# Optimization experiments

Measured on AMD Instinct MI355X. Metric: run time of the kernel, lower is better.

The kernel has to match this reference:

```python
import jax, jax.numpy as jnp
import numpy as np
from jax import lax

B, S, E, H = 8, 1024, 1024, 16
HEAD_DIM = E // H
THRESHOLD = 0.5
NEG_FILL = -1e9


def setup_inputs() -> dict:
    key = jax.random.key(0)
    k0, k1, k2 = jax.random.split(key, 3)
    x = jax.random.normal(k0, (B, S, E), jnp.float32)
    in_proj_w = jax.random.normal(k1, (3 * E, E), jnp.float32) * 0.02
    in_proj_b = jnp.zeros((3 * E,), jnp.float32)
    out_proj_w = jax.random.normal(k2, (E, E), jnp.float32) * 0.02
    out_proj_b = jnp.zeros((E,), jnp.float32)
    return {"x": x, "in_proj_w": in_proj_w, "in_proj_b": in_proj_b,
            "out_proj_w": out_proj_w, "out_proj_b": out_proj_b}


def _mha(x, in_proj_w, in_proj_b, out_proj_w, out_proj_b):
    # PyTorch nn.MultiheadAttention with q=k=v=x, batch_first=True
    qkv = x @ in_proj_w.T + in_proj_b                     # [B,S,3E]
    q, k, v = jnp.split(qkv, 3, axis=-1)                  # each [B,S,E]
    def split_heads(t):
        return t.reshape(B, S, H, HEAD_DIM).transpose(0, 2, 1, 3)  # [B,H,S,d]
    q, k, v = split_heads(q), split_heads(k), split_heads(v)
    scale = 1.0 / np.sqrt(HEAD_DIM).astype(np.float32)
    scores = jnp.einsum('bhqd,bhkd->bhqk', q, k) * scale  # [B,H,S,S]
    w = jax.nn.softmax(scores, axis=-1)
    o = jnp.einsum('bhqk,bhkd->bhqd', w, v)               # [B,H,S,d]
    o = o.transpose(0, 2, 1, 3).reshape(B, S, E)
    attn_output = o @ out_proj_w.T + out_proj_b           # [B,S,E]
    attn_weights = w.mean(axis=1)                         # head-averaged [B,S,S]
    return attn_output, attn_weights


def _cluster(attn_weights):
    # Sequential greedy clustering: scan rows i in order; if row i is not yet
    # visited, its high-attention columns (> THRESHOLD) form cluster i and are
    # marked visited. cluster_id[b, j] = row index of the first cluster that
    # claimed token j, or -1 if never claimed.
    visited0 = jnp.zeros((B, S), dtype=bool)
    cid0 = jnp.full((B, S), -1, dtype=jnp.int32)

    def step(carry, i):
        visited, cid = carry
        process = ~jnp.take(visited, i, axis=1)           # [B] row i unvisited?
        high = jnp.take(attn_weights, i, axis=1) > THRESHOLD  # [B,S]
        claimed = process[:, None] & high                 # [B,S]
        newly = claimed & (~visited)
        cid = jnp.where(newly, jnp.int32(i), cid)
        visited = visited | claimed
        return (visited, cid), None

    (visited, cid), _ = lax.scan(step, (visited0, cid0), jnp.arange(S))
    return cid, visited


def reference(x, in_proj_w, in_proj_b, out_proj_w, out_proj_b):
    attn_output, attn_weights = _mha(x, in_proj_w, in_proj_b, out_proj_w, out_proj_b)
    cluster_ids, covered = _cluster(attn_weights)
    # _generate_image_features: x where token belongs to some cluster, -1e9 else
    clustered_outputs = jnp.where(covered[..., None], x, jnp.float32(NEG_FILL))
    return attn_output, attn_weights, clustered_outputs, cluster_ids
```

## Files before the change

kernel.cpp:

```cpp
#include <hip/hip_runtime.h>
#include <hip/hip_bf16.h>

#define B 8
#define S 1024
#define E 1024
#define H 16

typedef unsigned short u16;
typedef unsigned char u8;
typedef unsigned int u32;
typedef unsigned long long u64;

typedef __attribute__((ext_vector_type(8))) short s16x8;
typedef __attribute__((ext_vector_type(4))) float f32x4;
typedef __attribute__((ext_vector_type(16))) float f32x16;

__device__ __forceinline__ float bf2f(u16 u) {
    union { u32 i; float f; } x; x.i = ((u32)u) << 16; return x.f;
}
__device__ __forceinline__ u16 f2bf(float f) {
    union { float f; u32 i; } x; x.f = f;
    u32 r = x.i + 0x7FFFu + ((x.i >> 16) & 1u);
    return (u16)(r >> 16);
}
__device__ __forceinline__ f32x16 zero16() {
    f32x16 z;
#pragma unroll
    for (int i = 0; i < 16; ++i) z[i] = 0.f;
    return z;
}
__device__ __forceinline__ void gload16(const u16* g, u16* l) {
    __builtin_amdgcn_global_load_lds(
        (const __attribute__((address_space(1))) u32*)g,
        (__attribute__((address_space(3))) u32*)l, 16, 0, 0);
}

__global__ __launch_bounds__(256) void cvt_all(
    const float* __restrict__ x, const float* __restrict__ w0,
    const float* __restrict__ w1, u16* __restrict__ xb,
    u16* __restrict__ wb0, u16* __restrict__ wb1) {
    int i = blockIdx.x * 256 + threadIdx.x;
    const float* src;
    u16* dst;
    int off;
    if (i < 2097152) { src = x; dst = xb; off = i; }
    else if (i < 2883584) { src = w0; dst = wb0; off = i - 2097152; }
    else { src = w1; dst = wb1; off = i - 2883584; }
    float4 v = ((const float4*)src)[off];
    union { u16 u[4]; ushort4 s; } p;
    p.u[0] = f2bf(v.x); p.u[1] = f2bf(v.y);
    p.u[2] = f2bf(v.z); p.u[3] = f2bf(v.w);
    ((ushort4*)dst)[off] = p.s;
}

template <int MODE>
__global__ __launch_bounds__(256) void mfma_gemm(
    const u16* __restrict__ A, const u16* __restrict__ W,
    const float* __restrict__ bias, u16* __restrict__ qb, u16* __restrict__ kb,
    u16* __restrict__ vt, float* __restrict__ outf) {
    __shared__ __align__(16) u16 smem[16384];
    u16* As = smem;
    u16* Bs = smem + 8192;
    const int t = threadIdx.x;
    const int lane = t & 63;
    const int w = t >> 6;
    const int lin = (int)(blockIdx.y * gridDim.x + blockIdx.x);
    const int xcd = lin & 7;
    const int idx = lin >> 3;
    int mt, nt;
    if (MODE == 0) { mt = (xcd & 3) * 16 + (idx & 15); nt = (xcd >> 2) * 12 + (idx >> 4); }
    else           { mt = xcd * 8 + (idx & 7);         nt = idx >> 3; }
    const int m0 = mt * 128;
    const int n0 = nt * 128;
    const int wm = w >> 1, wn = w & 1;
    const int l15 = lane & 15, l4 = lane >> 4;
    const int lr = lane >> 3;
    const int lc = ((lane & 7) ^ lr) * 8;

    f32x4 acc[4][4];
#pragma unroll
    for (int i = 0; i < 4; ++i)
#pragma unroll
        for (int j = 0; j < 4; ++j) acc[i][j] = {0.f, 0.f, 0.f, 0.f};

    for (int k0 = 0; k0 < 1024; k0 += 64) {
        __syncthreads();
#pragma unroll
        for (int jj = 0; jj < 4; ++jj) {
            int j = w * 4 + jj;
            gload16(A + (size_t)(m0 + j * 8 + lr) * 1024 + k0 + lc, As + j * 512);
            gload16(W + (size_t)(n0 + j * 8 + lr) * 1024 + k0 + lc, Bs + j * 512);
        }
        __syncthreads();
#pragma unroll
        for (int ks = 0; ks < 2; ++ks) {
            s16x8 af[4], bf[4];
#pragma unroll
            for (int i = 0; i < 4; ++i) {
                int row = wm * 64 + i * 16 + l15;
                af[i] = *(const s16x8*)((const u8*)As +
                        (((row << 7) + (ks << 6) + (l4 << 4)) ^ ((row & 7) << 4)));
            }
#pragma unroll
            for (int j = 0; j < 4; ++j) {
                int row = wn * 64 + j * 16 + l15;
                bf[j] = *(const s16x8*)((const u8*)Bs +
                        (((row << 7) + (ks << 6) + (l4 << 4)) ^ ((row & 7) << 4)));
            }
#pragma unroll
            for (int i = 0; i < 4; ++i)
#pragma unroll
                for (int j = 0; j < 4; ++j)
                    acc[i][j] = __builtin_amdgcn_mfma_f32_16x16x32_bf16(
                        af[i], bf[j], acc[i][j], 0, 0, 0);
        }
    }

    if (MODE == 0) {
        __syncthreads();
        u16* Cs = smem;
        const int seg = n0 >> 10;
        const int bb = m0 >> 10;
        const int ms = m0 & 1023;
        if (seg < 2) {
            const float sc = (seg == 0) ? 0.18033688011f : 1.0f;
#pragma unroll
            for (int j = 0; j < 4; ++j) {
                int nl = wn * 64 + j * 16 + l15;
                float bn = bias[n0 + nl];
#pragma unroll
                for (int i = 0; i < 4; ++i) {
                    int ml = wm * 64 + i * 16 + l4 * 4;
#pragma unroll
                    for (int rr = 0; rr < 4; ++rr)
                        Cs[(ml + rr) * 128 + nl] = f2bf((acc[i][j][rr] + bn) * sc);
                }
            }
            __syncthreads();
            u16* dst0 = (seg == 0) ? qb : kb;
#pragma unroll
            for (int it = 0; it < 8; ++it) {
                int flat = it * 256 + t;
                int ml = flat >> 4;
                int g = (flat >> 3) & 1;
                int c8 = flat & 7;
                int hh = ((n0 + g * 64) & 1023) >> 6;
                u16* dst = dst0 + (((size_t)(bb * 16 + hh) * 1024 + ms + ml) << 6) + c8 * 8;
                *(uint4*)dst = *(const uint4*)(Cs + ml * 128 + g * 64 + c8 * 8);
            }
        } else {
#pragma unroll
            for (int j = 0; j < 4; ++j) {
                int nl = wn * 64 + j * 16 + l15;
                float bn = bias[n0 + nl];
                int sz = (nl & 7) << 4;
#pragma unroll
                for (int i = 0; i < 4; ++i) {
                    int ml = wm * 64 + i * 16 + l4 * 4;
#pragma unroll
                    for (int rr = 0; rr < 4; ++rr) {
                        int bl = (ml + rr) << 1;
                        *(u16*)((u8*)Cs + (nl << 8) + (bl ^ sz)) =
                            f2bf(acc[i][j][rr] + bn);
                    }
                }
            }
            __syncthreads();
#pragma unroll
            for (int it = 0; it < 8; ++it) {
                int flat = it * 256 + t;
                int nl = flat >> 4;
                int c = flat & 15;
                int n = n0 + nl;
                int hh = (n & 1023) >> 6;
                int d = n & 63;
                u16* dst = vt + ((size_t)(bb * 16 + hh) * 64 + d) * 1024 + ms + c * 8;
                *(uint4*)dst = *(const uint4*)((u8*)Cs + (nl << 8) +
                                               ((c << 4) ^ ((nl & 7) << 4)));
            }
        }
    } else {
#pragma unroll
        for (int j = 0; j < 4; ++j) {
            int n = n0 + wn * 64 + j * 16 + l15;
            float bn = bias[n];
#pragma unroll
            for (int i = 0; i < 4; ++i) {
                int mbase = m0 + wm * 64 + i * 16 + l4 * 4;
#pragma unroll
                for (int rr = 0; rr < 4; ++rr)
                    outf[(size_t)(mbase + rr) * 1024 + n] = acc[i][j][rr] + bn;
            }
        }
    }
}

template <int BASE>
__device__ __forceinline__ s16x8 build_pa(f32x16 e) {
    u32 a, bv, c, d;
    asm("v_cvt_pk_bf16_f32 %0, %1, %2" : "=v"(a) : "v"(e[BASE + 0]), "v"(e[BASE + 1]));
    asm("v_cvt_pk_bf16_f32 %0, %1, %2" : "=v"(bv) : "v"(e[BASE + 2]), "v"(e[BASE + 3]));
    asm("v_cvt_pk_bf16_f32 %0, %1, %2" : "=v"(c) : "v"(e[BASE + 4]), "v"(e[BASE + 5]));
    asm("v_cvt_pk_bf16_f32 %0, %1, %2" : "=v"(d) : "v"(e[BASE + 6]), "v"(e[BASE + 7]));
    asm("v_permlane32_swap_b32 %0, %1" : "+v"(a), "+v"(c));
    asm("v_permlane32_swap_b32 %0, %1" : "+v"(bv), "+v"(d));
    union { u32 w[4]; s16x8 v; } u;
    u.w[0] = a; u.w[1] = bv; u.w[2] = c; u.w[3] = d;
    return u.v;
}
__device__ __forceinline__ float pair_max(float v) {
    float a_ = v, b_ = v;
    asm("v_permlane32_swap_b32 %0, %1" : "+v"(a_), "+v"(b_));
    return fmaxf(a_, b_);
}
__device__ __forceinline__ float pair_sum(float v) {
    float a_ = v, b_ = v;
    asm("v_permlane32_swap_b32 %0, %1" : "+v"(a_), "+v"(b_));
    return a_ + b_;
}
__device__ __forceinline__ u32 pair_or(u32 v) {
    u32 a_ = v, b_ = v;
    asm("v_permlane32_swap_b32 %0, %1" : "+v"(a_), "+v"(b_));
    return a_ | b_;
}

__global__ __launch_bounds__(256, 4) void attn_flash(
    const u16* __restrict__ qg, const u16* __restrict__ kg,
    const u16* __restrict__ vtg, u16* __restrict__ og,
    float* __restrict__ stats) {
    __shared__ __align__(16) u16 bufK[2][64 * 64];
    __shared__ __align__(16) u16 bufV[2][64 * 64];
    const int t = threadIdx.x;
    const int lane = t & 63;
    const int w = t >> 6;
    const int task = ((blockIdx.x & 7) << 7) | (blockIdx.x >> 3);
    const int b = task >> 7;
    const int h = (task >> 3) & 15;
    const int qg_ = task & 7;
    const int q = lane & 31;
    const int hi = lane >> 5;
    const int q0 = qg_ * 128 + w * 32;
    const size_t hb = (size_t)(b * 16 + h) << 16;

    const int lr = lane >> 3;
    const int lc = ((lane & 7) ^ lr) * 8;
    const int swz = (q & 7) << 4;

#define STAGE(tt, bb)                                                          \
    do {                                                                       \
        _Pragma("unroll") for (int jj = 0; jj < 2; ++jj) {                     \
            int j = w * 2 + jj;                                                \
            gload16(kg + hb + (size_t)((tt) * 64 + j * 8 + lr) * 64 + lc,      \
                    bufK[bb] + j * 512);                                       \
            gload16(vtg + hb + (size_t)(j * 8 + lr) * 1024 + (tt) * 64 + lc,   \
                    bufV[bb] + j * 512);                                       \
        }                                                                      \
    } while (0)

    s16x8 qf[4];
#pragma unroll
    for (int s = 0; s < 4; ++s)
        qf[s] = *(const s16x8*)(qg + hb + (size_t)(q0 + q) * 64 + s * 16 + hi * 8);

    f32x16 oLo = zero16(), oHi = zero16();
    float m = -1e30f, l = 0.f;

    STAGE(0, 0);
    __syncthreads();
    int cur = 0;

    for (int tile = 0; tile < 16; ++tile) {
        if (tile < 15) STAGE(tile + 1, cur ^ 1);
        const u16* bK = bufK[cur];
        const u16* bV = bufV[cur];
#pragma unroll
        for (int kk = 0; kk < 64; kk += 32) {
            s16x8 ka[4];
#pragma unroll
            for (int s = 0; s < 4; ++s)
                ka[s] = *(const s16x8*)((const u8*)bK +
                        ((((kk + q) << 7) + (s << 5) + (hi << 4)) ^ swz));
            f32x16 s_ = zero16();
#pragma unroll
            for (int s = 0; s < 4; ++s)
                s_ = __builtin_amdgcn_mfma_f32_32x32x16_bf16(ka[s], qf[s], s_, 0, 0, 0);
            float m0 = fmaxf(fmaxf(s_[0], s_[4]), fmaxf(s_[8], s_[12]));
            float m1 = fmaxf(fmaxf(s_[1], s_[5]), fmaxf(s_[9], s_[13]));
            float m2 = fmaxf(fmaxf(s_[2], s_[6]), fmaxf(s_[10], s_[14]));
            float m3 = fmaxf(fmaxf(s_[3], s_[7]), fmaxf(s_[11], s_[15]));
            float pmax = pair_max(fmaxf(fmaxf(m0, m1), fmaxf(m2, m3)));
            if (__any(pmax > m + 11.5f)) {
                float mn = fmaxf(m, pmax);
                float r = exp2f(m - mn);
                m = mn;
                l *= r;
                oLo = oLo * r;
                oHi = oHi * r;
            }
            float s0 = 0.f, s1 = 0.f, s2 = 0.f, s3 = 0.f;
#pragma unroll
            for (int i = 0; i < 16; i += 4) {
                s_[i + 0] = exp2f(s_[i + 0] - m);
                s_[i + 1] = exp2f(s_[i + 1] - m);
                s_[i + 2] = exp2f(s_[i + 2] - m);
                s_[i + 3] = exp2f(s_[i + 3] - m);
                s0 += s_[i + 0]; s1 += s_[i + 1]; s2 += s_[i + 2]; s3 += s_[i + 3];
            }
            l += pair_sum((s0 + s1) + (s2 + s3));
            s16x8 p0 = build_pa<0>(s_), p1 = build_pa<8>(s_);
            s16x8 vLo0 = *(const s16x8*)((const u8*)bV +
                         (((q << 7) + (kk << 1) + (hi << 4)) ^ swz));
            s16x8 vLo1 = *(const s16x8*)((const u8*)bV +
                         (((q << 7) + (kk << 1) + 32 + (hi << 4)) ^ swz));
            s16x8 vHi0 = *(const s16x8*)((const u8*)bV +
                         ((((q + 32) << 7) + (kk << 1) + (hi << 4)) ^ swz));
            s16x8 vHi1 = *(const s16x8*)((const u8*)bV +
                         ((((q + 32) << 7) + (kk << 1) + 32 + (hi << 4)) ^ swz));
            oLo = __builtin_amdgcn_mfma_f32_32x32x16_bf16(vLo0, p0, oLo, 0, 0, 0);
            oLo = __builtin_amdgcn_mfma_f32_32x32x16_bf16(vLo1, p1, oLo, 0, 0, 0);
            oHi = __builtin_amdgcn_mfma_f32_32x32x16_bf16(vHi0, p0, oHi, 0, 0, 0);
            oHi = __builtin_amdgcn_mfma_f32_32x32x16_bf16(vHi1, p1, oHi, 0, 0, 0);
        }
        __syncthreads();
        cur ^= 1;
    }
#undef STAGE
    float inv = 1.0f / l;
    oLo = oLo * inv;
    oHi = oHi * inv;
    u16* orow = og + (size_t)(b * 1024 + q0 + q) * 1024 + h * 64;
#pragma unroll
    for (int rg = 0; rg < 4; ++rg) {
        union { u16 u[4]; u64 v; } pk;
#pragma unroll
        for (int j = 0; j < 4; ++j) pk.u[j] = f2bf(oLo[4 * rg + j]);
        *(u64*)(orow + 8 * rg + 4 * hi) = pk.v;
#pragma unroll
        for (int j = 0; j < 4; ++j) pk.u[j] = f2bf(oHi[4 * rg + j]);
        *(u64*)(orow + 32 + 4 * hi + 8 * rg) = pk.v;
    }
    if (hi == 0)
        stats[(size_t)(b * 16 + h) * 1024 + q0 + q] = m + 4.0f + log2f(l);
}

__global__ __launch_bounds__(512, 2) void attn_aw(
    const u16* __restrict__ qg, const u16* __restrict__ kg,
    const float* __restrict__ stats, float* __restrict__ aw,
    u64* __restrict__ maskg) {
    __shared__ __align__(16) u16 bufK[2][128 * 64];
    __shared__ __align__(16) u16 bufQ[2][128 * 64];
    const int t = threadIdx.x;
    const int lane = t & 63;
    const int w = t >> 6;
    const int task = ((blockIdx.x & 7) << 6) | (blockIdx.x >> 3);
    const int b = task >> 6;
    const int ks = (task >> 3) & 7;
    const int qg_ = task & 7;
    const int q = lane & 31;
    const int hi = lane >> 5;
    const int wq = w >> 1;
    const int kh = w & 1;
    const int q0 = qg_ * 128;
    const int qr = wq * 32 + q;
    const int krow0 = kh * 64;
    const int kbase = ks * 128 + kh * 64;

    const int lr = lane >> 3;
    const int lc = ((lane & 7) ^ lr) * 8;
    const int swz = (q & 7) << 4;

#define STAGEAW(hh, bb)                                                        \
    do {                                                                       \
        const size_t hbs = (size_t)(b * 16 + (hh)) << 16;                      \
        _Pragma("unroll") for (int jj = 0; jj < 2; ++jj) {                     \
            int j = w * 2 + jj;                        \
            gload16(kg + hbs + (size_t)(ks * 128 + j * 8 + lr) * 64 + lc,      \
                    bufK[bb] + j * 512);                                       \
            gload16(qg + hbs + (size_t)(q0 + j * 8 + lr) * 64 + lc,            \
                    bufQ[bb] + j * 512);                                       \
        }                                                                      \
    } while (0)

    f32x16 awA = zero16(), awB = zero16();

    STAGEAW(0, 0);
    __syncthreads();
    int cur = 0;

    for (int h = 0; h < 16; ++h) {
        if (h < 15) STAGEAW(h + 1, cur ^ 1);
        const u16* bK = bufK[cur];
        const u16* bQ = bufQ[cur];
        s16x8 qf[4], kA[4], kB[4];
#pragma unroll
        for (int s = 0; s < 4; ++s) {
            qf[s] = *(const s16x8*)((const u8*)bQ +
                    (((qr << 7) + (s << 5) + (hi << 4)) ^ swz));
            kA[s] = *(const s16x8*)((const u8*)bK +
                    ((((krow0 + q) << 7) + (s << 5) + (hi << 4)) ^ swz));
            kB[s] = *(const s16x8*)((const u8*)bK +
                    ((((krow0 + q + 32) << 7) + (s << 5) + (hi << 4)) ^ swz));
        }
        float C = stats[(size_t)(b * 16 + h) * 1024 + q0 + qr];
        f32x16 sA = zero16(), sB = zero16();
#pragma unroll
        for (int s = 0; s < 4; ++s) {
            sA = __builtin_amdgcn_mfma_f32_32x32x16_bf16(kA[s], qf[s], sA, 0, 0, 0);
            sB = __builtin_amdgcn_mfma_f32_32x32x16_bf16(kB[s], qf[s], sB, 0, 0, 0);
        }
#pragma unroll
        for (int i = 0; i < 16; ++i) {
            awA[i] += exp2f(sA[i] - C);
            awB[i] += exp2f(sB[i] - C);
        }
        __syncthreads();
        cur ^= 1;
    }
#undef STAGEAW
    float* awrow = aw + (size_t)(b * 1024 + q0 + qr) * 1024 + kbase;
#pragma unroll
    for (int rg = 0; rg < 4; ++rg) {
        *(float4*)(awrow + 8 * rg + 4 * hi) =
            make_float4(awA[4 * rg + 0], awA[4 * rg + 1], awA[4 * rg + 2], awA[4 * rg + 3]);
        *(float4*)(awrow + 32 + 8 * rg + 4 * hi) =
            make_float4(awB[4 * rg + 0], awB[4 * rg + 1], awB[4 * rg + 2], awB[4 * rg + 3]);
    }
    u32 lo = 0, hi32 = 0;
#pragma unroll
    for (int r = 0; r < 16; ++r) {
        int k = (r & 3) + 8 * (r >> 2) + 4 * hi;
        lo |= (awA[r] > 0.5f) ? (1u << k) : 0u;
        hi32 |= (awB[r] > 0.5f) ? (1u << k) : 0u;
    }
    lo = pair_or(lo);
    hi32 = pair_or(hi32);
    if (hi == 0)
        maskg[(size_t)(b * 1024 + q0 + qr) * 16 + ks * 2 + kh] =
            ((u64)hi32 << 32) | (u64)lo;
}

__global__ __launch_bounds__(256) void cluster_kernel(
    const u64* __restrict__ maskg, float* __restrict__ cid, u64* __restrict__ cov) {
    __shared__ u64 mask[16384];
    __shared__ u16 rows[1024];
    const int t = threadIdx.x;
    const int b = blockIdx.x;
#pragma unroll
    for (int i = 0; i < 64; ++i)
        mask[t + 256 * i] = maskg[(size_t)b * 16384 + t + 256 * i];
#pragma unroll
    for (int i = 0; i < 4; ++i) cid[b * S + t + 256 * i] = -1.0f;
    __syncthreads();
    if (t < 64) {
        int nr = 0;
        for (int it = 0; it < 16; ++it) {
            int row = it * 64 + t;
            const u64* mp = mask + row * 16;
            u64 orv = 0;
#pragma unroll
            for (int j = 0; j < 16; ++j) orv |= mp[j];
            u64 bal = __ballot(orv != 0ULL);
            int pre = __popcll(bal & ((1ULL << t) - 1ULL));
            if (orv != 0ULL) rows[nr + pre] = (u16)row;
            nr += __popcll(bal);
        }
        u64 vis = 0;
        for (int idx = 0; idx < nr; ++idx) {
            int i = rows[idx];
            u64 viw = __shfl(vis, i >> 6);
            bool proc = ((viw >> (i & 63)) & 1ULL) == 0ULL;
            u64 cl = (proc && t < 16) ? mask[i * 16 + t] : 0ULL;
            u64 newly = cl & ~vis;
            vis |= cl;
            while (newly) {
                int bit = __ffsll((long long)newly) - 1;
                cid[b * S + t * 64 + bit] = (float)i;
                newly &= newly - 1;
            }
        }
        if (t < 16) cov[b * 16 + t] = vis;
    }
}

__global__ __launch_bounds__(256) void clustered_kernel(
    const float* __restrict__ x, const u64* __restrict__ cov,
    float* __restrict__ out2) {
    const size_t n4 = (size_t)B * S * E / 4;
    size_t idx = (size_t)blockIdx.x * 256 + threadIdx.x;
    const float4 neg = make_float4(-1e9f, -1e9f, -1e9f, -1e9f);
    for (; idx < n4; idx += (size_t)gridDim.x * 256) {
        size_t tok = idx >> 8;
        int bb = (int)(tok >> 10), s = (int)(tok & 1023);
        u64 m = cov[bb * 16 + (s >> 6)];
        bool c = ((m >> (s & 63)) & 1ULL) != 0ULL;
        float4 v = ((const float4*)x)[idx];
        ((float4*)out2)[idx] = c ? v : neg;
    }
}

extern "C" void kernel_launch(void* const* d_in, const int* in_sizes, int n_in,
                              void* d_out, int out_size, void* d_ws, size_t ws_size,
                              hipStream_t stream) {
    const float* x = (const float*)d_in[0];
    const float* w_in = (const float*)d_in[1];
    const float* b_in = (const float*)d_in[2];
    const float* w_out = (const float*)d_in[3];
    const float* b_out = (const float*)d_in[4];

    float* out0 = (float*)d_out;
    float* out1 = out0 + 8388608;
    float* out2 = out1 + 8388608;
    float* out3 = out2 + 8388608;

    u16* q_bf = (u16*)out0;
    u16* vt_bf = q_bf + 8388608;
    u16* xb = (u16*)out1;
    u16* k_bf = (u16*)out2;
    u16* wb0 = k_bf + 8388608;
    u16* wb1 = wb0 + 3145728;
    float* statsF = (float*)(k_bf + 12582912);
    u16* o_bf = (u16*)d_ws;
    u64* maskg = (u64*)((char*)d_ws + (size_t)(16u << 20));
    u64* cov = (u64*)((char*)d_ws + (size_t)(17u << 20));

    cvt_all<<<12288, 256, 0, stream>>>(x, w_in, w_out, xb, wb0, wb1);

    mfma_gemm<0><<<dim3(64, 24), 256, 0, stream>>>(xb, wb0, b_in, q_bf, k_bf,
                                                   vt_bf, nullptr);
    attn_flash<<<1024, 256, 0, stream>>>(q_bf, k_bf, vt_bf, o_bf, statsF);
    attn_aw<<<512, 512, 0, stream>>>(q_bf, k_bf, statsF, out1, maskg);
    mfma_gemm<1><<<dim3(64, 8), 256, 0, stream>>>(o_bf, wb1, b_out, nullptr,
                                                  nullptr, nullptr, out0);

    cluster_kernel<<<8, 256, 0, stream>>>(maskg, out3, cov);
    clustered_kernel<<<2048, 256, 0, stream>>>(x, cov, out2);
}
```

Baseline: 258.8 us.

## Fold max subtraction into MFMA init, sum softmax via ones-MFMA, stage GEMM output

The attention kernel now seeds the QK^T accumulator with -m, so the max subtraction comes out of the MFMA for free. The row sum l is computed by an extra pair of MFMAs against a ones vector instead of VALU adds and a permlane reduction. Separately, the fp32 output-projection epilogue is staged through shared memory and written as coalesced float4 rows, and the GEMM tile-to-block mapping is reordered. The trade-offs are extra MFMA work and extra barriers in the epilogue, and the row sum is now taken over the bf16-rounded probabilities.

New measurement: 258.6 us. Within noise of the previous version (-0.1%).

```diff
diff --git a/kernel.cpp b/kernel.cpp
--- a/kernel.cpp
+++ b/kernel.cpp
@@ -68,8 +68,8 @@
     const int xcd = lin & 7;
     const int idx = lin >> 3;
     int mt, nt;
-    if (MODE == 0) { mt = (xcd & 3) * 16 + (idx & 15); nt = (xcd >> 2) * 12 + (idx >> 4); }
-    else           { mt = xcd * 8 + (idx & 7);         nt = idx >> 3; }
+    if (MODE == 0) { mt = (xcd & 3) * 16 + idx / 12; nt = (xcd >> 2) * 12 + idx % 12; }
+    else           { mt = xcd * 8 + idx / 8;         nt = idx % 8; }
     const int m0 = mt * 128;
     const int n0 = nt * 128;
     const int wm = w >> 1, wn = w & 1;
@@ -180,17 +180,34 @@
             }
         }
     } else {
-#pragma unroll
-        for (int j = 0; j < 4; ++j) {
-            int n = n0 + wn * 64 + j * 16 + l15;
-            float bn = bias[n];
-#pragma unroll
-            for (int i = 0; i < 4; ++i) {
-                int mbase = m0 + wm * 64 + i * 16 + l4 * 4;
-#pragma unroll
-                for (int rr = 0; rr < 4; ++rr)
-                    outf[(size_t)(mbase + rr) * 1024 + n] = acc[i][j][rr] + bn;
-            }
+        __syncthreads();
+        float* Csf = (float*)smem;
+#pragma unroll
+        for (int r = 0; r < 2; ++r) {
+            if (wm == r) {
+#pragma unroll
+                for (int j = 0; j < 4; ++j) {
+                    int nl = wn * 64 + j * 16 + l15;
+                    float bn = bias[n0 + nl];
+#pragma unroll
+                    for (int i = 0; i < 4; ++i) {
+                        int mlr = i * 16 + l4 * 4;
+#pragma unroll
+                        for (int rr = 0; rr < 4; ++rr)
+                            Csf[(mlr + rr) * 128 + nl] = acc[i][j][rr] + bn;
+                    }
+                }
+            }
+            __syncthreads();
+#pragma unroll
+            for (int it = 0; it < 8; ++it) {
+                int flat = it * 256 + t;
+                int row = flat >> 5;
+                int c4 = flat & 31;
+                *(float4*)(outf + (size_t)(m0 + r * 64 + row) * 1024 + n0 + c4 * 4) =
+                    *(const float4*)(Csf + row * 128 + c4 * 4);
+            }
+            __syncthreads();
         }
     }
 }
@@ -212,11 +229,6 @@
     float a_ = v, b_ = v;
     asm("v_permlane32_swap_b32 %0, %1" : "+v"(a_), "+v"(b_));
     return fmaxf(a_, b_);
-}
-__device__ __forceinline__ float pair_sum(float v) {
-    float a_ = v, b_ = v;
-    asm("v_permlane32_swap_b32 %0, %1" : "+v"(a_), "+v"(b_));
-    return a_ + b_;
 }
 __device__ __forceinline__ u32 pair_or(u32 v) {
     u32 a_ = v, b_ = v;
@@ -246,6 +258,11 @@
     const int lc = ((lane & 7) ^ lr) * 8;
     const int swz = (q & 7) << 4;
 
+    union { u32 wd[4]; s16x8 v; } onesu;
+    onesu.wd[0] = 0x3F803F80u; onesu.wd[1] = 0x3F803F80u;
+    onesu.wd[2] = 0x3F803F80u; onesu.wd[3] = 0x3F803F80u;
+    const s16x8 ones = onesu.v;
+
 #define STAGE(tt, bb)                                                          \
     do {                                                                       \
         _Pragma("unroll") for (int jj = 0; jj < 2; ++jj) {                     \
@@ -262,8 +279,8 @@
     for (int s = 0; s < 4; ++s)
         qf[s] = *(const s16x8*)(qg + hb + (size_t)(q0 + q) * 64 + s * 16 + hi * 8);
 
-    f32x16 oLo = zero16(), oHi = zero16();
-    float m = -1e30f, l = 0.f;
+    f32x16 oLo = zero16(), oHi = zero16(), lacc = zero16();
+    float m = 0.f;
 
     STAGE(0, 0);
     __syncthreads();
@@ -280,7 +297,10 @@
             for (int s = 0; s < 4; ++s)
                 ka[s] = *(const s16x8*)((const u8*)bK +
                         ((((kk + q) << 7) + (s << 5) + (hi << 4)) ^ swz));
-            f32x16 s_ = zero16();
+            f32x16 s_;
+            const float negm = -m;
+#pragma unroll
+            for (int i = 0; i < 16; ++i) s_[i] = negm;
 #pragma unroll
             for (int s = 0; s < 4; ++s)
                 s_ = __builtin_amdgcn_mfma_f32_32x32x16_bf16(ka[s], qf[s], s_, 0, 0, 0);
@@ -288,26 +308,22 @@
             float m1 = fmaxf(fmaxf(s_[1], s_[5]), fmaxf(s_[9], s_[13]));
             float m2 = fmaxf(fmaxf(s_[2], s_[6]), fmaxf(s_[10], s_[14]));
             float m3 = fmaxf(fmaxf(s_[3], s_[7]), fmaxf(s_[11], s_[15]));
-            float pmax = pair_max(fmaxf(fmaxf(m0, m1), fmaxf(m2, m3)));
-            if (__any(pmax > m + 11.5f)) {
-                float mn = fmaxf(m, pmax);
-                float r = exp2f(m - mn);
-                m = mn;
-                l *= r;
+            float padj = pair_max(fmaxf(fmaxf(m0, m1), fmaxf(m2, m3)));
+            if (__any(padj > 11.5f)) {
+                float delta = fmaxf(padj, 0.f);
+                float r = exp2f(-delta);
+                m += delta;
+                lacc[0] *= r;
                 oLo = oLo * r;
                 oHi = oHi * r;
-            }
-            float s0 = 0.f, s1 = 0.f, s2 = 0.f, s3 = 0.f;
-#pragma unroll
-            for (int i = 0; i < 16; i += 4) {
-                s_[i + 0] = exp2f(s_[i + 0] - m);
-                s_[i + 1] = exp2f(s_[i + 1] - m);
-                s_[i + 2] = exp2f(s_[i + 2] - m);
-                s_[i + 3] = exp2f(s_[i + 3] - m);
-                s0 += s_[i + 0]; s1 += s_[i + 1]; s2 += s_[i + 2]; s3 += s_[i + 3];
-            }
-            l += pair_sum((s0 + s1) + (s2 + s3));
+#pragma unroll
+                for (int i = 0; i < 16; ++i) s_[i] -= delta;
+            }
+#pragma unroll
+            for (int i = 0; i < 16; ++i) s_[i] = exp2f(s_[i]);
             s16x8 p0 = build_pa<0>(s_), p1 = build_pa<8>(s_);
+            lacc = __builtin_amdgcn_mfma_f32_32x32x16_bf16(ones, p0, lacc, 0, 0, 0);
+            lacc = __builtin_amdgcn_mfma_f32_32x32x16_bf16(ones, p1, lacc, 0, 0, 0);
             s16x8 vLo0 = *(const s16x8*)((const u8*)bV +
                          (((q << 7) + (kk << 1) + (hi << 4)) ^ swz));
             s16x8 vLo1 = *(const s16x8*)((const u8*)bV +
@@ -325,6 +341,7 @@
         cur ^= 1;
     }
 #undef STAGE
+    const float l = lacc[0];
     float inv = 1.0f / l;
     oLo = oLo * inv;
     oHi = oHi * inv;
@@ -373,7 +390,7 @@
     do {                                                                       \
         const size_t hbs = (size_t)(b * 16 + (hh)) << 16;                      \
         _Pragma("unroll") for (int jj = 0; jj < 2; ++jj) {                     \
-            int j = w * 2 + jj;                        \
+            int j = w * 2 + jj;                                                \
             gload16(kg + hbs + (size_t)(ks * 128 + j * 8 + lr) * 64 + lc,      \
                     bufK[bb] + j * 512);                                       \
             gload16(qg + hbs + (size_t)(q0 + j * 8 + lr) * 64 + lc,            \
```
